# Kernel tuning notes

Measured on AMD Instinct MI355X. Metric: run time of the kernel, lower is better.

## Reference

```python
import jax, jax.numpy as jnp
import numpy as np


def setup_inputs() -> dict:
    key = jax.random.key(0)
    k1, k2, k3, k4 = jax.random.split(key, 4)
    H = W = 1024
    B = 16
    image = jax.random.normal(k1, (1, H, W), dtype=jnp.float32)
    x = jax.random.normal(k2, (B, 1, H, W), dtype=jnp.float32)
    # Conv2d(1, 9, 3) parameters, torch layout: weight (out=9, in=1, 3, 3), bias (9,)
    fan_in = 1 * 3 * 3
    bound = 1.0 / np.sqrt(fan_in)
    W_KL = jax.random.uniform(k3, (9, 1, 3, 3), jnp.float32, -bound, bound)
    b_KL = jax.random.uniform(k4, (9,), jnp.float32, -bound, bound)
    return {"image": image, "x": x, "W_KL": W_KL, "b_KL": b_KL}


def reference(image, x, W_KL, b_KL):
    # K = Conv2d(image): (1,H,W) -> (9,H,W), 'same' padding
    K = jax.lax.conv_general_dilated(
        image[None], W_KL, window_strides=(1, 1), padding='SAME',
        dimension_numbers=('NCHW', 'OIHW', 'NCHW'))[0] + b_KL[:, None, None]
    H, W = image.shape[1], image.shape[2]
    # permute (9,H,W) -> (H,W,9) -> unflatten to per-pixel 3x3 kernels (H,W,3,3)
    K = jnp.transpose(K, (1, 2, 0)).reshape(H, W, 3, 3)
    # Apply spatially-varying 3x3 kernel: y[b,c,h,w] = sum_{a,d} K[h,w,a,d] * x_pad[b,c,h+a,w+d]
    x_pad = jnp.pad(x, ((0, 0), (0, 0), (1, 1), (1, 1)))
    y = jnp.zeros_like(x)
    for a in range(3):
        for d in range(3):
            y = y + K[:, :, a, d] * x_pad[:, :, a:a + H, d:d + W]
    return y
```

## Files before the change

kernel.cpp:

```cpp
#include <hip/hip_runtime.h>

#define IH 1024
#define IW 1024
#define NB 16
#define NB2 8

typedef float v4f __attribute__((ext_vector_type(4)));

#define VMWAIT(n) asm volatile("s_waitcnt vmcnt(" #n ")" ::: "memory")

__device__ __forceinline__ void glds16(const float* g, float* l) {
    __builtin_amdgcn_global_load_lds(
        (const __attribute__((address_space(1))) void*)g,
        (__attribute__((address_space(3))) void*)l, 16, 0, 0);
}

struct RawWin { v4f mv[3]; float fl[3]; float fr[3]; };

__device__ __forceinline__ void issue_win(const float* __restrict__ plane,
                                          int h, int w0, RawWin& rw) {
#pragma unroll
    for (int a = 0; a < 3; ++a) {
        const int hh = h + a - 1;
        const int hc = (hh < 0) ? 0 : (hh >= IH ? IH - 1 : hh);
        const float* rowp = plane + (size_t)hc * IW;
        rw.fl[a] = rowp[w0 > 0 ? w0 - 1 : 0];
        rw.mv[a] = *(const v4f*)(rowp + w0);
        rw.fr[a] = rowp[w0 + 4 < IW ? w0 + 4 : IW - 1];
    }
}

__device__ __forceinline__ void fin_win_img(const RawWin& rw, int h, int w0,
                                            float win[3][6]) {
#pragma unroll
    for (int a = 0; a < 3; ++a) {
        const int hh = h + a - 1;
        const bool rowok = (hh >= 0) & (hh < IH);
        win[a][0] = (rowok && w0 > 0)      ? rw.fl[a]   : 0.f;
        win[a][1] = rowok ? rw.mv[a].x : 0.f;
        win[a][2] = rowok ? rw.mv[a].y : 0.f;
        win[a][3] = rowok ? rw.mv[a].z : 0.f;
        win[a][4] = rowok ? rw.mv[a].w : 0.f;
        win[a][5] = (rowok && w0 + 4 < IW) ? rw.fr[a]   : 0.f;
    }
}

__global__ __launch_bounds__(256, 4) void fused_z8(
    const float* __restrict__ image,
    const float* __restrict__ x,
    const float* __restrict__ Wk,
    const float* __restrict__ bk,
    float* __restrict__ out)
{
    __shared__ float lds[2][6][256];

    const int tx = threadIdx.x;
    const int wv = threadIdx.y;

    const int hwid  = blockIdx.x;
    const int xcd   = hwid & 7;
    const int chunk = hwid >> 3;
    const int bz    = chunk & 1;
    const int bx    = (chunk >> 1) & 3;
    const int g     = xcd * 32 + (chunk >> 3);
    const int c0    = bx * 256;
    const int h0    = g * 4;
    const int h     = h0 + wv;
    const int lc    = tx * 4;
    const int w0    = c0 + lc;
    const int b0    = bz * NB2;

    const size_t plane = (size_t)IH * IW;

    int zv; asm("v_mov_b32 %0, 0" : "=v"(zv));

    auto stage = [&](int gb, int buf) {
        const float* xb = x + (size_t)gb * plane;
        int gr = h0 - 1 + wv; gr = gr < 0 ? 0 : gr;
        glds16(xb + (size_t)gr * IW + c0 + tx * 4, &lds[buf][wv][0]);
        if (wv < 2) {
            int g2 = h0 + 3 + wv; g2 = g2 > IH - 1 ? IH - 1 : g2;
            glds16(xb + (size_t)g2 * IW + c0 + tx * 4, &lds[buf][wv + 4][0]);
        }
    };
    auto halo = [&](int gb, float* HL, float* HR) {
        const float* xb = x + (size_t)gb * plane;
        const int cl = (c0 > 0) ? c0 - 1 : 0;
        const int cr = (c0 + 256 < IW) ? c0 + 256 : IW - 1;
#pragma unroll
        for (int a = 0; a < 3; ++a) {
            int gr = h + a - 1; gr = gr < 0 ? 0 : (gr > IH - 1 ? IH - 1 : gr);
            const float* rp = xb + (size_t)gr * IW;
            HL[a] = rp[cl + zv];
            HR[a] = rp[cr + zv];
        }
    };

    RawWin rimg;
    issue_win(image, h, w0, rimg);
    stage(b0, 0);
    float hl[2][3], hr[2][3];
    halo(b0, hl[0], hr[0]);

    float wkk[81];
#pragma unroll
    for (int i = 0; i < 81; ++i) wkk[i] = Wk[i];
    float bb[9];
#pragma unroll
    for (int c = 0; c < 9; ++c) bb[c] = bk[c];

    float p[3][6];
    fin_win_img(rimg, h, w0, p);
    float Kv[4][9];
#pragma unroll
    for (int j = 0; j < 4; ++j)
#pragma unroll
        for (int c = 0; c < 9; ++c) {
            float acc = bb[c];
#pragma unroll
            for (int a = 0; a < 3; ++a)
#pragma unroll
                for (int d = 0; d < 3; ++d)
                    acc = fmaf(wkk[c * 9 + a * 3 + d], p[a][j + d], acc);
            Kv[j][c] = acc;
        }
    {
        const bool top = (h == 0);
        const bool bot = (h == IH - 1);
#pragma unroll
        for (int j = 0; j < 4; ++j)
#pragma unroll
            for (int d = 0; d < 3; ++d) {
                Kv[j][d]     = top ? 0.f : Kv[j][d];
                Kv[j][6 + d] = bot ? 0.f : Kv[j][6 + d];
            }
    }

    VMWAIT(6);
    __builtin_amdgcn_sched_barrier(0);
    __builtin_amdgcn_s_barrier();
    __builtin_amdgcn_sched_barrier(0);

    v4f yprev;
    float* obp = out + (size_t)h * IW + w0;
    const int ll = (tx > 0)  ? lc - 4 : 0;
    const int lr = (tx < 63) ? lc + 4 : 252;

#pragma unroll
    for (int b = 0; b < NB2; ++b) {
        const int gb = b0 + b;
        if (b > 0)
            __builtin_nontemporal_store(yprev,
                                        (v4f*)(obp + (size_t)(gb - 1) * plane));
        if (b + 1 < NB2) {
            stage(gb + 1, (b + 1) & 1);
            halo(gb + 1, hl[(b + 1) & 1], hr[(b + 1) & 1]);
        }
        {
            const float* lb = &lds[b & 1][0][0];
            float win[3][6];
#pragma unroll
            for (int a = 0; a < 3; ++a) {
                const float* rowp = lb + (wv + a) * 256;
                const v4f lv = *(const v4f*)(rowp + ll);
                const v4f mv = *(const v4f*)(rowp + lc);
                const v4f rv = *(const v4f*)(rowp + lr);
                const float le = (tx == 0)  ? hl[b & 1][a] : lv.w;
                const float re = (tx == 63) ? hr[b & 1][a] : rv.x;
                win[a][0] = (w0 > 0)      ? le : 0.f;
                win[a][1] = mv.x; win[a][2] = mv.y;
                win[a][3] = mv.z; win[a][4] = mv.w;
                win[a][5] = (w0 + 4 < IW) ? re : 0.f;
            }
            v4f yy;
#pragma unroll
            for (int j = 0; j < 4; ++j) {
                float acc = 0.f;
#pragma unroll
                for (int a = 0; a < 3; ++a)
#pragma unroll
                    for (int d = 0; d < 3; ++d)
                        acc = fmaf(Kv[j][a * 3 + d], win[a][j + d], acc);
                yy[j] = acc;
            }
            yprev = yy;
        }
        if (b + 1 < NB2) {
            VMWAIT(6);
            __builtin_amdgcn_sched_barrier(0);
            __builtin_amdgcn_s_barrier();
            __builtin_amdgcn_sched_barrier(0);
        }
    }
    __builtin_nontemporal_store(yprev,
                                (v4f*)(obp + (size_t)(b0 + NB2 - 1) * plane));
}

extern "C" void kernel_launch(void* const* d_in, const int* in_sizes, int n_in,
                              void* d_out, int out_size, void* d_ws, size_t ws_size,
                              hipStream_t stream) {
    const float* image = (const float*)d_in[0];
    const float* x     = (const float*)d_in[1];
    const float* Wk    = (const float*)d_in[2];
    const float* bk    = (const float*)d_in[3];
    float* out = (float*)d_out;

    dim3 block(64, 4);
    dim3 grid(2048);
    fused_z8<<<grid, block, 0, stream>>>(image, x, Wk, bk, out);
}
```

Measured before the change: 130.8 us.

## Deepen LDS staging pipeline from double to triple buffering

Raises the shared-memory ring from two to three buffers so each iteration prefetches the batch two steps ahead, and issues two stages up front. The vmcnt waits are re-tuned per iteration and per wave (waves that issue extra rows wait on different counts), with sched barriers added to fix issue order. The goal is to hide more global-load latency behind compute. In exchange it uses more LDS and registers for halo values, and it relies on hand-counted waitcnt values that must exactly match the issued loads.

```diff
diff --git a/kernel.cpp b/kernel.cpp
--- a/kernel.cpp
+++ b/kernel.cpp
@@ -8,6 +8,7 @@
 typedef float v4f __attribute__((ext_vector_type(4)));
 
 #define VMWAIT(n) asm volatile("s_waitcnt vmcnt(" #n ")" ::: "memory")
+#define SCHEDB()  __builtin_amdgcn_sched_barrier(0)
 
 __device__ __forceinline__ void glds16(const float* g, float* l) {
     __builtin_amdgcn_global_load_lds(
@@ -45,14 +46,14 @@
     }
 }
 
-__global__ __launch_bounds__(256, 4) void fused_z8(
+__global__ __launch_bounds__(256, 4) void fused_d3(
     const float* __restrict__ image,
     const float* __restrict__ x,
     const float* __restrict__ Wk,
     const float* __restrict__ bk,
     float* __restrict__ out)
 {
-    __shared__ float lds[2][6][256];
+    __shared__ float lds[3][6][256];
 
     const int tx = threadIdx.x;
     const int wv = threadIdx.y;
@@ -98,9 +99,12 @@
 
     RawWin rimg;
     issue_win(image, h, w0, rimg);
-    stage(b0, 0);
-    float hl[2][3], hr[2][3];
-    halo(b0, hl[0], hr[0]);
+    SCHEDB();
+    float hl[3][3], hr[3][3];
+    stage(b0, 0);                 SCHEDB();
+    halo(b0, hl[0], hr[0]);       SCHEDB();
+    stage(b0 + 1, 1);             SCHEDB();
+    halo(b0 + 1, hl[1], hr[1]);   SCHEDB();
 
     float wkk[81];
 #pragma unroll
@@ -136,10 +140,10 @@
             }
     }
 
-    VMWAIT(6);
-    __builtin_amdgcn_sched_barrier(0);
+    if (wv < 2) { VMWAIT(14); } else { VMWAIT(13); }
+    SCHEDB();
     __builtin_amdgcn_s_barrier();
-    __builtin_amdgcn_sched_barrier(0);
+    SCHEDB();
 
     v4f yprev;
     float* obp = out + (size_t)h * IW + w0;
@@ -149,15 +153,17 @@
 #pragma unroll
     for (int b = 0; b < NB2; ++b) {
         const int gb = b0 + b;
-        if (b > 0)
+        if (b > 0) {
             __builtin_nontemporal_store(yprev,
                                         (v4f*)(obp + (size_t)(gb - 1) * plane));
-        if (b + 1 < NB2) {
-            stage(gb + 1, (b + 1) & 1);
-            halo(gb + 1, hl[(b + 1) & 1], hr[(b + 1) & 1]);
+            SCHEDB();
+        }
+        if (b + 2 < NB2) {
+            stage(gb + 2, (b + 2) % 3);                      SCHEDB();
+            halo(gb + 2, hl[(b + 2) % 3], hr[(b + 2) % 3]);  SCHEDB();
         }
         {
-            const float* lb = &lds[b & 1][0][0];
+            const float* lb = &lds[b % 3][0][0];
             float win[3][6];
 #pragma unroll
             for (int a = 0; a < 3; ++a) {
@@ -165,8 +171,8 @@
                 const v4f lv = *(const v4f*)(rowp + ll);
                 const v4f mv = *(const v4f*)(rowp + lc);
                 const v4f rv = *(const v4f*)(rowp + lr);
-                const float le = (tx == 0)  ? hl[b & 1][a] : lv.w;
-                const float re = (tx == 63) ? hr[b & 1][a] : rv.x;
+                const float le = (tx == 0)  ? hl[b % 3][a] : lv.w;
+                const float re = (tx == 63) ? hr[b % 3][a] : rv.x;
                 win[a][0] = (w0 > 0)      ? le : 0.f;
                 win[a][1] = mv.x; win[a][2] = mv.y;
                 win[a][3] = mv.z; win[a][4] = mv.w;
@@ -186,10 +192,12 @@
             yprev = yy;
         }
         if (b + 1 < NB2) {
-            VMWAIT(6);
-            __builtin_amdgcn_sched_barrier(0);
+            if (b == 0)      { if (wv < 2) { VMWAIT(14); } else { VMWAIT(13); } }
+            else if (b == 6) { VMWAIT(7); }
+            else             { if (wv < 2) { VMWAIT(15); } else { VMWAIT(14); } }
+            SCHEDB();
             __builtin_amdgcn_s_barrier();
-            __builtin_amdgcn_sched_barrier(0);
+            SCHEDB();
         }
     }
     __builtin_nontemporal_store(yprev,
@@ -207,5 +215,5 @@
 
     dim3 block(64, 4);
     dim3 grid(2048);
-    fused_z8<<<grid, block, 0, stream>>>(image, x, Wk, bk, out);
-}
+    fused_d3<<<grid, block, 0, stream>>>(image, x, Wk, bk, out);
+}
```

Result: no change. 129.2 us (-1.2%).
